# Optimization experiments

Hardware: AMD Instinct MI355X
Metric: run time of the kernel (lower is better)

## Reference

```python
import jax, jax.numpy as jnp
import numpy as np


def setup_inputs() -> dict:
    key = jax.random.key(0)
    k1, k2 = jax.random.split(key)
    x = jax.random.normal(k1, (16384, 1024), dtype=jnp.float32)
    # 10 butterfly stages, each with 512 independent 2x2 mixing matrices
    Ws = jax.random.normal(k2, (10, 512, 2, 2), dtype=jnp.float32)
    return {"x": x, "Ws": Ws}


def reference(x, Ws):
    """PairLinear_MixerBlock forward for input_dim == output_dim == 2^L.
    selector and reducer are Identity; only the butterfly mixing stages remain.
    """
    bs, dim = x.shape
    n_stages = Ws.shape[0]  # log2(dim)
    y = x
    for i in range(n_stages):
        stride = 2 ** i
        # y.view(-1, 2, 2**i).permute(0, 2, 1).contiguous().view(bs, -1)
        y = y.reshape(-1, 2, stride).transpose(0, 2, 1).reshape(bs, -1)
        # PairLinear: view(bs, -1, 2) then per-pair 2x2 matmul with Ws[i]
        y = jnp.einsum('bpk,pkj->bpj', y.reshape(bs, -1, 2), Ws[i]).reshape(bs, -1)
        # y.view(-1, 2**i, 2).permute(0, 2, 1).contiguous()
        y = y.reshape(-1, stride, 2).transpose(0, 2, 1).reshape(bs, dim)
    return y
```

## Files before the change

### kernel.cpp

```cpp
#include <hip/hip_runtime.h>

#define DIM 1024
#define ROWS_PER_TILE 16

typedef float  f32x4  __attribute__((ext_vector_type(4)));
typedef short  bf16x8 __attribute__((ext_vector_type(8)));
typedef unsigned int u32x2 __attribute__((ext_vector_type(2)));
typedef unsigned int u32x4 __attribute__((ext_vector_type(4)));

#define WF_BYTES (2 * 32 * 2 * 64 * 16)


__device__ __forceinline__ short f2bfs(float f) {
    union { __bf16 b; short s; } c; c.b = (__bf16)f; return c.s;
}
__device__ __forceinline__ unsigned f2bfbits(float f) {
    union { __bf16 b; unsigned short u; } c; c.b = (__bf16)f; return (unsigned)c.u;
}
__device__ __forceinline__ float bfbits2f(unsigned bits16shifted) {
    union { unsigned u; float f; } c; c.u = bits16shifted; return c.f;
}

__global__ __launch_bounds__(64) void compose_pack(const float* __restrict__ Ws,
                                                   short* __restrict__ wf) {
    __shared__ float M[32 * 32];
    const int b = blockIdx.x;
    const int tid = threadIdx.x;
    const bool isB = b >= 32;
    const int grp = isB ? b - 32 : b;

    for (int s = tid; s < 1024; s += 64) M[s] = ((s >> 5) == (s & 31)) ? 1.f : 0.f;
    __syncthreads();

    for (int il = 0; il < 5; ++il) {
        #pragma unroll
        for (int s = 0; s < 8; ++s) {
            int task = tid + s * 64;
            int pl = task >> 5;
            int r  = task & 31;
            int lo = ((pl >> il) << (il + 1)) | (pl & ((1 << il) - 1));
            int hi = lo + (1 << il);
            int wi = isB ? ((5 + il) * 512 + pl * 32 + grp)
                         : (il * 512 + grp * 16 + pl);
            const float* W = Ws + (size_t)wi * 4;
            float w00 = W[0], w01 = W[1], w10 = W[2], w11 = W[3];
            float u = M[r * 32 + lo], v = M[r * 32 + hi];
            M[r * 32 + lo] = u * w00 + v * w10;
            M[r * 32 + hi] = u * w01 + v * w11;
        }
        __syncthreads();
    }

    const int q = tid >> 4, lr = tid & 15;
    #pragma unroll
    for (int nh = 0; nh < 2; ++nh) {
        bf16x8 fr;
        #pragma unroll
        for (int e = 0; e < 8; ++e)
            fr[e] = f2bfs(M[(q * 8 + e) * 32 + nh * 16 + lr]);
        size_t idx = (size_t)(isB ? 4096 : 0) + ((size_t)grp * 2 + nh) * 64 + tid;
        ((bf16x8*)wf)[idx] = fr;
    }
}

__global__ __launch_bounds__(256) void bfly_mfma(
    const float* __restrict__ x,
    const short* __restrict__ wf1,
    const short* __restrict__ wf2,
    float* __restrict__ out)
{
    __shared__ char zt[32 * 1024];
    const int tid = threadIdx.x;
    const int w = tid >> 6;
    const int l = tid & 63;
    const int q = l >> 4, lr = l & 15;
    const int row0 = blockIdx.x * ROWS_PER_TILE;

    const f32x4 zacc = {0.f, 0.f, 0.f, 0.f};

    const float* xrow = x + (size_t)(row0 + lr) * DIM;
    #pragma unroll
    for (int gi = 0; gi < 8; ++gi) {
        const int g = w * 8 + gi;
        const f32x4* xp = (const f32x4*)(xrow + g * 32 + q * 8);
        f32x4 xa = __builtin_nontemporal_load(xp);
        f32x4 xb = __builtin_nontemporal_load(xp + 1);
        bf16x8 af;
        af[0] = f2bfs(xa[0]); af[1] = f2bfs(xa[1]);
        af[2] = f2bfs(xa[2]); af[3] = f2bfs(xa[3]);
        af[4] = f2bfs(xb[0]); af[5] = f2bfs(xb[1]);
        af[6] = f2bfs(xb[2]); af[7] = f2bfs(xb[3]);
        bf16x8 b0 = ((const bf16x8*)wf1)[(g * 2 + 0) * 64 + l];
        bf16x8 b1 = ((const bf16x8*)wf1)[(g * 2 + 1) * 64 + l];
        f32x4 c0 = __builtin_amdgcn_mfma_f32_16x16x32_bf16(af, b0, zacc, 0, 0, 0);
        f32x4 c1 = __builtin_amdgcn_mfma_f32_16x16x32_bf16(af, b1, zacc, 0, 0, 0);
        #pragma unroll
        for (int nh = 0; nh < 2; ++nh) {
            f32x4 cc = nh ? c1 : c0;
            int c = nh * 16 + lr;
            unsigned lo = f2bfbits(cc[0]) | (f2bfbits(cc[1]) << 16);
            unsigned hi = f2bfbits(cc[2]) | (f2bfbits(cc[3]) << 16);
            int byteoff = (c * 1024 + g * 32 + q * 8) ^ ((c & 15) << 3);
            u32x2 pk = {lo, hi};
            *(u32x2*)(zt + byteoff) = pk;
        }
    }
    __syncthreads();

    f32x4 o[2][8];
    #pragma unroll
    for (int hh = 0; hh < 8; ++hh) {
        const int h = w * 8 + hh;
        bf16x8 a2;
        #pragma unroll
        for (int e = 0; e < 8; ++e) {
            int byteoff = (h * 1024 + (q * 8 + e) * 32 + lr * 2) ^ ((h & 15) << 3);
            union { unsigned short u; short s; } cv;
            cv.u = *(const unsigned short*)(zt + byteoff);
            a2[e] = cv.s;
        }
        bf16x8 b0 = ((const bf16x8*)wf2)[(h * 2 + 0) * 64 + l];
        bf16x8 b1 = ((const bf16x8*)wf2)[(h * 2 + 1) * 64 + l];
        o[0][hh] = __builtin_amdgcn_mfma_f32_16x16x32_bf16(b0, a2, zacc, 0, 0, 0);
        o[1][hh] = __builtin_amdgcn_mfma_f32_16x16x32_bf16(b1, a2, zacc, 0, 0, 0);
    }
    __syncthreads();

    #pragma unroll
    for (int nh = 0; nh < 2; ++nh) {
        #pragma unroll
        for (int i = 0; i < 4; ++i) {
            unsigned p0 = f2bfbits(o[nh][0][i]) | (f2bfbits(o[nh][1][i]) << 16);
            unsigned p1 = f2bfbits(o[nh][2][i]) | (f2bfbits(o[nh][3][i]) << 16);
            unsigned p2 = f2bfbits(o[nh][4][i]) | (f2bfbits(o[nh][5][i]) << 16);
            unsigned p3 = f2bfbits(o[nh][6][i]) | (f2bfbits(o[nh][7][i]) << 16);
            int colb = (nh * 16 + q * 4 + i) * 32 + w * 8;
            int u = lr * 128 + (colb >> 3);
            u ^= (u >> 7) & 7;
            u32x4 pk = {p0, p1, p2, p3};
            *(u32x4*)(zt + u * 16) = pk;
        }
    }
    __syncthreads();

    const int trow = tid >> 4;
    const int tcb  = tid & 15;
    float* orow = out + (size_t)(row0 + trow) * DIM;
    #pragma unroll
    for (int j = 0; j < 8; ++j) {
        int ucol = j * 16 + tcb;
        int u = trow * 128 + ucol;
        u ^= (u >> 7) & 7;
        u32x4 pk = *(const u32x4*)(zt + u * 16);
        f32x4 v0, v1;
        v0[0] = bfbits2f(pk[0] << 16); v0[1] = bfbits2f(pk[0] & 0xffff0000u);
        v0[2] = bfbits2f(pk[1] << 16); v0[3] = bfbits2f(pk[1] & 0xffff0000u);
        v1[0] = bfbits2f(pk[2] << 16); v1[1] = bfbits2f(pk[2] & 0xffff0000u);
        v1[2] = bfbits2f(pk[3] << 16); v1[3] = bfbits2f(pk[3] & 0xffff0000u);
        float* dst = orow + ucol * 8;
        *(f32x4*)dst = v0;
        *((f32x4*)dst + 1) = v1;
    }
}

__global__ __launch_bounds__(256) void butterfly_fallback(
    const float* __restrict__ x, const float* __restrict__ Ws,
    float* __restrict__ out, int rows)
{
    const int lane = threadIdx.x & 63;
    const int wave = threadIdx.x >> 6;
    const int row0 = (blockIdx.x * 4 + wave) * 2;
    const float4* __restrict__ Wm = (const float4*)Ws;
    float d[2][16];
    #pragma unroll
    for (int r = 0; r < 2; ++r) {
        int row = row0 + r;
        if (row < rows) {
            const f32x4* src = (const f32x4*)(x + (size_t)row * DIM);
            #pragma unroll
            for (int qq = 0; qq < 4; ++qq) {
                f32x4 v = src[qq * 64 + lane];
                d[r][qq*4+0]=v[0]; d[r][qq*4+1]=v[1]; d[r][qq*4+2]=v[2]; d[r][qq*4+3]=v[3];
            }
        } else { for (int e = 0; e < 16; ++e) d[r][e] = 0.f; }
    }
    #pragma unroll
    for (int qq = 0; qq < 4; ++qq) {
        int base = qq*128 + lane*2;
        float4 m0 = Wm[base], m1 = Wm[base+1];
        #pragma unroll
        for (int r = 0; r < 2; ++r) {
            int e = qq*4; float u,v;
            u=d[r][e+0]; v=d[r][e+1]; d[r][e+0]=u*m0.x+v*m0.z; d[r][e+1]=u*m0.y+v*m0.w;
            u=d[r][e+2]; v=d[r][e+3]; d[r][e+2]=u*m1.x+v*m1.z; d[r][e+3]=u*m1.y+v*m1.w;
        }
    }
    #pragma unroll
    for (int qq = 0; qq < 4; ++qq) {
        int base = 512 + qq*128 + lane*2;
        float4 m0 = Wm[base], m1 = Wm[base+1];
        #pragma unroll
        for (int r = 0; r < 2; ++r) {
            int e = qq*4; float u,v;
            u=d[r][e+0]; v=d[r][e+2]; d[r][e+0]=u*m0.x+v*m0.z; d[r][e+2]=u*m0.y+v*m0.w;
            u=d[r][e+1]; v=d[r][e+3]; d[r][e+1]=u*m1.x+v*m1.z; d[r][e+3]=u*m1.y+v*m1.w;
        }
    }
    #pragma unroll
    for (int i = 2; i < 8; ++i) {
        const int m = 1 << (i - 2);
        #pragma unroll
        for (int qq = 0; qq < 4; ++qq) {
            const int a = (lane >> (i - 2)) & 1;
            int P0 = (((qq*64 + lane) >> (i-1)) << i) | ((lane & (m-1)) << 2);
            int base = i*512 + P0;
            float4 M0 = Wm[base+0], M1 = Wm[base+1], M2 = Wm[base+2], M3 = Wm[base+3];
            float wA0 = a ? M0.w : M0.x, wB0 = a ? M0.y : M0.z;
            float wA1 = a ? M1.w : M1.x, wB1 = a ? M1.y : M1.z;
            float wA2 = a ? M2.w : M2.x, wB2 = a ? M2.y : M2.z;
            float wA3 = a ? M3.w : M3.x, wB3 = a ? M3.y : M3.z;
            #pragma unroll
            for (int r = 0; r < 2; ++r) {
                int e = qq*4;
                float o0=__shfl_xor(d[r][e+0],m), o1=__shfl_xor(d[r][e+1],m);
                float o2=__shfl_xor(d[r][e+2],m), o3=__shfl_xor(d[r][e+3],m);
                d[r][e+0]=d[r][e+0]*wA0+o0*wB0; d[r][e+1]=d[r][e+1]*wA1+o1*wB1;
                d[r][e+2]=d[r][e+2]*wA2+o2*wB2; d[r][e+3]=d[r][e+3]*wA3+o3*wB3;
            }
        }
    }
    #pragma unroll
    for (int qp = 0; qp < 2; ++qp) {
        int base = 8*512 + qp*256 + lane*4;
        float4 M0 = Wm[base+0], M1 = Wm[base+1], M2 = Wm[base+2], M3 = Wm[base+3];
        #pragma unroll
        for (int r = 0; r < 2; ++r) {
            int eu=(2*qp)*4, ev=(2*qp+1)*4; float u,v;
            u=d[r][eu+0]; v=d[r][ev+0]; d[r][eu+0]=u*M0.x+v*M0.z; d[r][ev+0]=u*M0.y+v*M0.w;
            u=d[r][eu+1]; v=d[r][ev+1]; d[r][eu+1]=u*M1.x+v*M1.z; d[r][ev+1]=u*M1.y+v*M1.w;
            u=d[r][eu+2]; v=d[r][ev+2]; d[r][eu+2]=u*M2.x+v*M2.z; d[r][ev+2]=u*M2.y+v*M2.w;
            u=d[r][eu+3]; v=d[r][ev+3]; d[r][eu+3]=u*M3.x+v*M3.z; d[r][ev+3]=u*M3.y+v*M3.w;
        }
    }
    #pragma unroll
    for (int qp = 0; qp < 2; ++qp) {
        int base = 9*512 + qp*256 + lane*4;
        float4 M0 = Wm[base+0], M1 = Wm[base+1], M2 = Wm[base+2], M3 = Wm[base+3];
        #pragma unroll
        for (int r = 0; r < 2; ++r) {
            int eu=qp*4, ev=(qp+2)*4; float u,v;
            u=d[r][eu+0]; v=d[r][ev+0]; d[r][eu+0]=u*M0.x+v*M0.z; d[r][ev+0]=u*M0.y+v*M0.w;
            u=d[r][eu+1]; v=d[r][ev+1]; d[r][eu+1]=u*M1.x+v*M1.z; d[r][ev+1]=u*M1.y+v*M1.w;
            u=d[r][eu+2]; v=d[r][ev+2]; d[r][eu+2]=u*M2.x+v*M2.z; d[r][ev+2]=u*M2.y+v*M2.w;
            u=d[r][eu+3]; v=d[r][ev+3]; d[r][eu+3]=u*M3.x+v*M3.z; d[r][ev+3]=u*M3.y+v*M3.w;
        }
    }
    #pragma unroll
    for (int r = 0; r < 2; ++r) {
        int row = row0 + r;
        if (row < rows) {
            f32x4* dst = (f32x4*)(out + (size_t)row * DIM);
            #pragma unroll
            for (int qq = 0; qq < 4; ++qq) {
                f32x4 v = { d[r][qq*4+0], d[r][qq*4+1], d[r][qq*4+2], d[r][qq*4+3] };
                dst[qq * 64 + lane] = v;
            }
        }
    }
}

extern "C" void kernel_launch(void* const* d_in, const int* in_sizes, int n_in,
                              void* d_out, int out_size, void* d_ws, size_t ws_size,
                              hipStream_t stream) {
    const float* x  = (const float*)d_in[0];
    const float* Ws = (const float*)d_in[1];
    float* out = (float*)d_out;
    int rows = in_sizes[0] / DIM;

    if (ws_size >= (size_t)WF_BYTES && (rows % ROWS_PER_TILE) == 0) {
        short* wf1 = (short*)d_ws;
        short* wf2 = (short*)d_ws + 32768;
        compose_pack<<<64, 64, 0, stream>>>(Ws, (short*)d_ws);
        bfly_mfma<<<rows / ROWS_PER_TILE, 256, 0, stream>>>(x, wf1, wf2, out);
    } else {
        int grid = (rows + 7) / 8;
        butterfly_fallback<<<grid, 256, 0, stream>>>(x, Ws, out, rows);
    }
}
```

Measured before the change: 46.53 us.

## Hoist x loads, drop a barrier, per-wave output staging, nontemporal stores

Issues all sixteen x vector loads up front so they are in flight together before the convert and MFMA loop. The final-stage output staging is reorganised into per-wave 8 KB LDS regions, which lets one __syncthreads be removed, and the global stores become nontemporal. compose_pack now runs four waves per block (16 blocks of 256) instead of 64 single-wave blocks. Preloading all of x raises register pressure, and the new LDS indexing must still map every column correctly.

```diff
diff --git a/kernel.cpp b/kernel.cpp
--- a/kernel.cpp
+++ b/kernel.cpp
@@ -21,21 +21,23 @@
     union { unsigned u; float f; } c; c.u = bits16shifted; return c.f;
 }
 
-__global__ __launch_bounds__(64) void compose_pack(const float* __restrict__ Ws,
-                                                   short* __restrict__ wf) {
-    __shared__ float M[32 * 32];
-    const int b = blockIdx.x;
-    const int tid = threadIdx.x;
+__global__ __launch_bounds__(256) void compose_pack(const float* __restrict__ Ws,
+                                                    short* __restrict__ wf) {
+    __shared__ float M[4][1024];
+    const int wave = threadIdx.x >> 6;
+    const int lane = threadIdx.x & 63;
+    const int b = blockIdx.x * 4 + wave;
     const bool isB = b >= 32;
     const int grp = isB ? b - 32 : b;
 
-    for (int s = tid; s < 1024; s += 64) M[s] = ((s >> 5) == (s & 31)) ? 1.f : 0.f;
+    for (int s = lane; s < 1024; s += 64)
+        M[wave][s] = ((s >> 5) == (s & 31)) ? 1.f : 0.f;
     __syncthreads();
 
     for (int il = 0; il < 5; ++il) {
         #pragma unroll
         for (int s = 0; s < 8; ++s) {
-            int task = tid + s * 64;
+            int task = lane + s * 64;
             int pl = task >> 5;
             int r  = task & 31;
             int lo = ((pl >> il) << (il + 1)) | (pl & ((1 << il) - 1));
@@ -44,21 +46,21 @@
                          : (il * 512 + grp * 16 + pl);
             const float* W = Ws + (size_t)wi * 4;
             float w00 = W[0], w01 = W[1], w10 = W[2], w11 = W[3];
-            float u = M[r * 32 + lo], v = M[r * 32 + hi];
-            M[r * 32 + lo] = u * w00 + v * w10;
-            M[r * 32 + hi] = u * w01 + v * w11;
+            float u = M[wave][r * 32 + lo], v = M[wave][r * 32 + hi];
+            M[wave][r * 32 + lo] = u * w00 + v * w10;
+            M[wave][r * 32 + hi] = u * w01 + v * w11;
         }
         __syncthreads();
     }
 
-    const int q = tid >> 4, lr = tid & 15;
+    const int q = lane >> 4, lr = lane & 15;
     #pragma unroll
     for (int nh = 0; nh < 2; ++nh) {
         bf16x8 fr;
         #pragma unroll
         for (int e = 0; e < 8; ++e)
-            fr[e] = f2bfs(M[(q * 8 + e) * 32 + nh * 16 + lr]);
-        size_t idx = (size_t)(isB ? 4096 : 0) + ((size_t)grp * 2 + nh) * 64 + tid;
+            fr[e] = f2bfs(M[wave][(q * 8 + e) * 32 + nh * 16 + lr]);
+        size_t idx = (size_t)(isB ? 4096 : 0) + ((size_t)grp * 2 + nh) * 64 + lane;
         ((bf16x8*)wf)[idx] = fr;
     }
 }
@@ -79,12 +81,18 @@
     const f32x4 zacc = {0.f, 0.f, 0.f, 0.f};
 
     const float* xrow = x + (size_t)(row0 + lr) * DIM;
+    f32x4 xv[16];
+    #pragma unroll
+    for (int gi = 0; gi < 8; ++gi) {
+        const f32x4* xp = (const f32x4*)(xrow + (w * 8 + gi) * 32 + q * 8);
+        xv[2 * gi]     = __builtin_nontemporal_load(xp);
+        xv[2 * gi + 1] = __builtin_nontemporal_load(xp + 1);
+    }
+
     #pragma unroll
     for (int gi = 0; gi < 8; ++gi) {
         const int g = w * 8 + gi;
-        const f32x4* xp = (const f32x4*)(xrow + g * 32 + q * 8);
-        f32x4 xa = __builtin_nontemporal_load(xp);
-        f32x4 xb = __builtin_nontemporal_load(xp + 1);
+        f32x4 xa = xv[2 * gi], xb = xv[2 * gi + 1];
         bf16x8 af;
         af[0] = f2bfs(xa[0]); af[1] = f2bfs(xa[1]);
         af[2] = f2bfs(xa[2]); af[3] = f2bfs(xa[3]);
@@ -124,7 +132,6 @@
         o[0][hh] = __builtin_amdgcn_mfma_f32_16x16x32_bf16(b0, a2, zacc, 0, 0, 0);
         o[1][hh] = __builtin_amdgcn_mfma_f32_16x16x32_bf16(b1, a2, zacc, 0, 0, 0);
     }
-    __syncthreads();
 
     #pragma unroll
     for (int nh = 0; nh < 2; ++nh) {
@@ -134,11 +141,10 @@
             unsigned p1 = f2bfbits(o[nh][2][i]) | (f2bfbits(o[nh][3][i]) << 16);
             unsigned p2 = f2bfbits(o[nh][4][i]) | (f2bfbits(o[nh][5][i]) << 16);
             unsigned p3 = f2bfbits(o[nh][6][i]) | (f2bfbits(o[nh][7][i]) << 16);
-            int colb = (nh * 16 + q * 4 + i) * 32 + w * 8;
-            int u = lr * 128 + (colb >> 3);
-            u ^= (u >> 7) & 7;
+            unsigned u = lr * 32 + (nh * 16 + q * 4 + i);
+            u ^= (u >> 5) & 7;
             u32x4 pk = {p0, p1, p2, p3};
-            *(u32x4*)(zt + u * 16) = pk;
+            *(u32x4*)(zt + w * 8192 + u * 16) = pk;
         }
     }
     __syncthreads();
@@ -147,19 +153,20 @@
     const int tcb  = tid & 15;
     float* orow = out + (size_t)(row0 + trow) * DIM;
     #pragma unroll
-    for (int j = 0; j < 8; ++j) {
-        int ucol = j * 16 + tcb;
-        int u = trow * 128 + ucol;
-        u ^= (u >> 7) & 7;
-        u32x4 pk = *(const u32x4*)(zt + u * 16);
+    for (int jp = 0; jp < 8; ++jp) {
+        int C = jp * 128 + tcb * 8;
+        int n = jp * 4 + (tcb >> 2);
+        int j = tcb & 3;
+        unsigned u = trow * 32 + n;
+        u ^= (u >> 5) & 7;
+        u32x4 pk = *(const u32x4*)(zt + j * 8192 + u * 16);
         f32x4 v0, v1;
         v0[0] = bfbits2f(pk[0] << 16); v0[1] = bfbits2f(pk[0] & 0xffff0000u);
         v0[2] = bfbits2f(pk[1] << 16); v0[3] = bfbits2f(pk[1] & 0xffff0000u);
         v1[0] = bfbits2f(pk[2] << 16); v1[1] = bfbits2f(pk[2] & 0xffff0000u);
         v1[2] = bfbits2f(pk[3] << 16); v1[3] = bfbits2f(pk[3] & 0xffff0000u);
-        float* dst = orow + ucol * 8;
-        *(f32x4*)dst = v0;
-        *((f32x4*)dst + 1) = v1;
+        __builtin_nontemporal_store(v0, (f32x4*)(orow + C));
+        __builtin_nontemporal_store(v1, (f32x4*)(orow + C) + 1);
     }
 }
 
@@ -280,7 +287,7 @@
     if (ws_size >= (size_t)WF_BYTES && (rows % ROWS_PER_TILE) == 0) {
         short* wf1 = (short*)d_ws;
         short* wf2 = (short*)d_ws + 32768;
-        compose_pack<<<64, 64, 0, stream>>>(Ws, (short*)d_ws);
+        compose_pack<<<16, 256, 0, stream>>>(Ws, (short*)d_ws);
         bfly_mfma<<<rows / ROWS_PER_TILE, 256, 0, stream>>>(x, wf1, wf2, out);
     } else {
         int grid = (rows + 7) / 8;
```

Result: slower. 56.52 us (+21.5%).
